# Optimization experiments

Hardware: AMD Instinct MI355X
Metric: run time of the kernel (lower is better)

Reference implementation:

```python
import jax, jax.numpy as jnp
import numpy as np

NUM_HEADS = 16


def _bayes_w(mu, rho, eps):
    # reparameterized weight sample: w = mu + softplus(rho) * eps
    return mu + jax.nn.softplus(rho) * eps


def setup_inputs() -> dict:
    key = jax.random.key(0)
    ks = jax.random.split(key, 12)
    B, N, C = 4, 2048, 1024
    x = jax.random.normal(ks[0], (B, N, C), jnp.float32)
    w_scale = 0.02
    q_w = jax.random.normal(ks[1], (C, C), jnp.float32) * w_scale
    k_w = jax.random.normal(ks[2], (C, C), jnp.float32) * w_scale
    v_mu = jax.random.normal(ks[3], (C, C), jnp.float32) * w_scale
    v_rho = jax.random.normal(ks[4], (C, C), jnp.float32) * 0.1 - 3.0
    v_eps = jax.random.normal(ks[5], (C, C), jnp.float32)
    proj_mu = jax.random.normal(ks[6], (C, C), jnp.float32) * w_scale
    proj_rho = jax.random.normal(ks[7], (C, C), jnp.float32) * 0.1 - 3.0
    proj_eps = jax.random.normal(ks[8], (C, C), jnp.float32)
    pb_mu = jax.random.normal(ks[9], (C,), jnp.float32) * w_scale
    pb_rho = jax.random.normal(ks[10], (C,), jnp.float32) * 0.1 - 3.0
    pb_eps = jax.random.normal(ks[11], (C,), jnp.float32)
    return {"x": x, "q_w": q_w, "k_w": k_w, "v_mu": v_mu, "v_rho": v_rho,
            "v_eps": v_eps, "proj_mu": proj_mu, "proj_rho": proj_rho,
            "proj_eps": proj_eps, "pb_mu": pb_mu, "pb_rho": pb_rho,
            "pb_eps": pb_eps}


def reference(x, q_w, k_w, v_mu, v_rho, v_eps, proj_mu, proj_rho, proj_eps,
              pb_mu, pb_rho, pb_eps):
    B, N, C = x.shape
    H = NUM_HEADS
    D = C // H
    scale = D ** -0.5
    v_w = _bayes_w(v_mu, v_rho, v_eps)
    # projections (torch Linear: y = x @ W.T)
    q = (x @ q_w.T).reshape(B, N, H, D).transpose(0, 2, 1, 3)  # [B,H,N,D]
    k = (x @ k_w.T).reshape(B, N, H, D).transpose(0, 2, 1, 3)
    v = (x @ v_w.T).reshape(B, N, H, D).transpose(0, 2, 1, 3)
    attn = jax.nn.softmax(jnp.einsum("bhnd,bhmd->bhnm", q * scale, k), axis=-1)
    out = jnp.einsum("bhnm,bhmd->bhnd", attn, v)
    out = out.transpose(0, 2, 1, 3).reshape(B, N, C)
    p_w = _bayes_w(proj_mu, proj_rho, proj_eps)
    p_b = _bayes_w(pb_mu, pb_rho, pb_eps)
    return out @ p_w.T + p_b
```

## Files before the change

kernel.cpp:

```cpp
#include <hip/hip_runtime.h>
#include <hip/hip_bf16.h>
#include <cstdint>
#include <math.h>

typedef __bf16 bf16;
typedef __bf16 bf16x8 __attribute__((ext_vector_type(8)));
typedef __bf16 bf16x4 __attribute__((ext_vector_type(4)));
typedef float  f32x4 __attribute__((ext_vector_type(4)));
typedef unsigned short u16x8 __attribute__((ext_vector_type(8)));

#define LOG2E 1.4426950408889634f

#define AS1 __attribute__((address_space(1)))
#define AS3 __attribute__((address_space(3)))

__device__ __forceinline__ void gload_lds16(const bf16* g, bf16* l) {
    __builtin_amdgcn_global_load_lds((AS1 void*)g, (AS3 void*)l, 16, 0, 0);
}

__device__ __forceinline__ float softplus(float r) {
    return (r > 15.f) ? r : log1pf(expf(r));
}

__global__ __launch_bounds__(256)
void cast_f32_bf16(const float* __restrict__ in, bf16* __restrict__ out, int n4) {
    int i = blockIdx.x * 256 + threadIdx.x;
    if (i < n4) {
        float4 v = ((const float4*)in)[i];
        bf16 o[4] = {(bf16)v.x, (bf16)v.y, (bf16)v.z, (bf16)v.w};
        *(uint64_t*)&out[i * 4] = *(uint64_t*)o;
    }
}

__global__ __launch_bounds__(256)
void wprep(const float* __restrict__ qw, const float* __restrict__ kw,
           const float* __restrict__ vmu, const float* __restrict__ vrho,
           const float* __restrict__ veps, bf16* __restrict__ wqkv) {
    int i = blockIdx.x * 256 + threadIdx.x;
    int r = blockIdx.y;
    float4 v;
    if (r == 0)      v = ((const float4*)qw)[i];
    else if (r == 1) v = ((const float4*)kw)[i];
    else {
        float4 m = ((const float4*)vmu)[i];
        float4 rh = ((const float4*)vrho)[i];
        float4 e = ((const float4*)veps)[i];
        v.x = m.x + softplus(rh.x) * e.x;
        v.y = m.y + softplus(rh.y) * e.y;
        v.z = m.z + softplus(rh.z) * e.z;
        v.w = m.w + softplus(rh.w) * e.w;
    }
    bf16 o[4] = {(bf16)v.x, (bf16)v.y, (bf16)v.z, (bf16)v.w};
    *(uint64_t*)&wqkv[((size_t)r << 20) + (size_t)i * 4] = *(uint64_t*)o;
}

__global__ __launch_bounds__(256)
void pprep(const float* __restrict__ pmu, const float* __restrict__ prho,
           const float* __restrict__ peps, const float* __restrict__ bmu,
           const float* __restrict__ brho, const float* __restrict__ beps,
           bf16* __restrict__ pwb, float* __restrict__ p_b) {
    int bx = blockIdx.x;
    if (bx < 1024) {
        int i = bx * 256 + threadIdx.x;
        float4 m = ((const float4*)pmu)[i];
        float4 rh = ((const float4*)prho)[i];
        float4 e = ((const float4*)peps)[i];
        bf16 o[4] = {(bf16)(m.x + softplus(rh.x) * e.x),
                     (bf16)(m.y + softplus(rh.y) * e.y),
                     (bf16)(m.z + softplus(rh.z) * e.z),
                     (bf16)(m.w + softplus(rh.w) * e.w)};
        *(uint64_t*)&pwb[(size_t)i * 4] = *(uint64_t*)o;
    } else {
        int i = threadIdx.x;
        float4 m = ((const float4*)bmu)[i];
        float4 rh = ((const float4*)brho)[i];
        float4 e = ((const float4*)beps)[i];
        float4 v = {m.x + softplus(rh.x) * e.x, m.y + softplus(rh.y) * e.y,
                    m.z + softplus(rh.z) * e.z, m.w + softplus(rh.w) * e.w};
        ((float4*)p_b)[i] = v;
    }
}

template <typename OutT>
__global__ __launch_bounds__(256)
void gemm_bt(const bf16* __restrict__ A, int lda, const bf16* __restrict__ W,
             OutT* __restrict__ C, int ldc, const float* __restrict__ bias,
             int M, int N, int K, float q_scale, int q_cols) {
    __shared__ bf16 lA[128 * 32];
    __shared__ bf16 lB[128 * 32];

    const int lane = threadIdx.x & 63;
    const int wv   = threadIdx.x >> 6;
    const int wr   = wv >> 1, wc = wv & 1;
    const int m0 = blockIdx.y * 128, n0 = blockIdx.x * 128;
    const int col = lane & 15, quad = lane >> 4;
    const float scale = (n0 < q_cols) ? q_scale : 1.0f;

    const int srow  = wv * 16 + (lane >> 2);
    const int skcol = (lane & 3) * 8;

    f32x4 acc[4][4] = {};

    for (int k0 = 0; k0 < K; k0 += 32) {
#pragma unroll
        for (int r = 0; r < 2; ++r) {
            gload_lds16(A + (size_t)(m0 + r * 64 + srow) * lda + k0 + skcol,
                        &lA[(r * 64 + wv * 16) * 32]);
            gload_lds16(W + (size_t)(n0 + r * 64 + srow) * K + k0 + skcol,
                        &lB[(r * 64 + wv * 16) * 32]);
        }
        __syncthreads();

        bf16x8 af[4], bfr[4];
#pragma unroll
        for (int t = 0; t < 4; ++t) {
            af[t]  = *(const bf16x8*)&lA[(wr * 64 + t * 16 + col) * 32 + quad * 8];
            bfr[t] = *(const bf16x8*)&lB[(wc * 64 + t * 16 + col) * 32 + quad * 8];
        }
#pragma unroll
        for (int i = 0; i < 4; ++i)
#pragma unroll
            for (int j = 0; j < 4; ++j)
                acc[i][j] = __builtin_amdgcn_mfma_f32_16x16x32_bf16(af[i], bfr[j], acc[i][j], 0, 0, 0);
        __syncthreads();
    }

#pragma unroll
    for (int i = 0; i < 4; ++i) {
        int row = m0 + wr * 64 + i * 16 + quad * 4;
#pragma unroll
        for (int j = 0; j < 4; ++j) {
            int cc = n0 + wc * 64 + j * 16 + col;
            float bv = bias ? bias[cc] : 0.f;
#pragma unroll
            for (int r = 0; r < 4; ++r)
                C[(size_t)(row + r) * ldc + cc] = (OutT)(acc[i][j][r] * scale + bv);
        }
    }
}

__global__ __launch_bounds__(256)
void vtrans(const bf16* __restrict__ QKV, bf16* __restrict__ Vt) {
    __shared__ uint32_t t[64 * 33];
    const int tid = threadIdx.x;
    const int kvt = blockIdx.x, h = blockIdx.y, b = blockIdx.z;
    const bf16* src = QKV + (size_t)(b * 2048 + kvt * 64) * 3072 + 2048 + h * 64;

    const int kp = tid >> 3, c = tid & 7;
    u16x8 v0 = *(const u16x8*)&src[(size_t)(2 * kp) * 3072 + c * 8];
    u16x8 v1 = *(const u16x8*)&src[(size_t)(2 * kp + 1) * 3072 + c * 8];
#pragma unroll
    for (int j = 0; j < 8; ++j)
        t[(c * 8 + j) * 33 + kp] = (uint32_t)v0[j] | ((uint32_t)v1[j] << 16);
    __syncthreads();

    const int d = tid >> 2, c2 = tid & 3;
    bf16* dst = &Vt[(size_t)((b * 16 + h) * 64 + d) * 2048 + kvt * 64 + c2 * 16];
    uint4 w0, w1;
    w0.x = t[d * 33 + c2 * 8 + 0];
    w0.y = t[d * 33 + c2 * 8 + 1];
    w0.z = t[d * 33 + c2 * 8 + 2];
    w0.w = t[d * 33 + c2 * 8 + 3];
    w1.x = t[d * 33 + c2 * 8 + 4];
    w1.y = t[d * 33 + c2 * 8 + 5];
    w1.z = t[d * 33 + c2 * 8 + 6];
    w1.w = t[d * 33 + c2 * 8 + 7];
    *(uint4*)dst       = w0;
    *(uint4*)(dst + 8) = w1;
}

__global__ __launch_bounds__(256, 3)
void attn_kernel(bf16* QKV, const bf16* __restrict__ Vt) {
    __shared__ bf16 sK[2][64 * 64];
    __shared__ bf16 sV[2][64 * 64];
    __shared__ bf16 sP[128 * 72];

    const int lane = threadIdx.x & 63;
    const int wv   = threadIdx.x >> 6;
    const int col  = lane & 15, quad = lane >> 4;
    const int qt = blockIdx.x, h = blockIdx.y, b = blockIdx.z;

    const size_t rowQ0 = (size_t)b * 2048 + qt * 128;
    bf16* Qg = QKV + rowQ0 * 3072 + h * 64;
    const bf16* Kg = QKV + (size_t)b * 2048 * 3072 + 1024 + h * 64;
    const bf16* Vg = Vt + (size_t)((b * 16 + h) * 64) * 2048;

    bf16x8 qf[2][2];
#pragma unroll
    for (int mi = 0; mi < 2; ++mi)
#pragma unroll
        for (int ks = 0; ks < 2; ++ks)
            qf[mi][ks] = *(const bf16x8*)&Qg[(size_t)(wv * 32 + mi * 16 + col) * 3072 + ks * 32 + quad * 8];

    const int rl = lane >> 3;
    const int cs = ((lane & 7) ^ rl) * 8;
    const bf16* Kdma = Kg + (size_t)(wv * 16 + rl) * 3072 + cs;
    const bf16* Vdma = Vg + (size_t)(wv * 16 + rl) * 2048 + cs;
    const int ldsrow = (wv * 16) * 64;

    gload_lds16(Kdma,                    &sK[0][ldsrow]);
    gload_lds16(Kdma + (size_t)8 * 3072, &sK[0][ldsrow + 8 * 64]);
    gload_lds16(Vdma,                    &sV[0][ldsrow]);
    gload_lds16(Vdma + (size_t)8 * 2048, &sV[0][ldsrow + 8 * 64]);

    f32x4 lsum[2] = {};
    f32x4 o[2][4] = {};
    const int cx = col & 7;

    for (int t = 0; t < 32; ++t) {
        __syncthreads();
        const int cur = t & 1;
        if (t < 31) {
            const int nxt = cur ^ 1;
            const size_t kvn = (size_t)(t + 1) * 64;
            gload_lds16(Kdma + kvn * 3072,       &sK[nxt][ldsrow]);
            gload_lds16(Kdma + (kvn + 8) * 3072, &sK[nxt][ldsrow + 8 * 64]);
            gload_lds16(Vdma + kvn,              &sV[nxt][ldsrow]);
            gload_lds16(Vdma + kvn + 8 * 2048,   &sV[nxt][ldsrow + 8 * 64]);
        }

        f32x4 st[2][4];
#pragma unroll
        for (int nj = 0; nj < 4; ++nj) {
            bf16x8 kf0 = *(const bf16x8*)&sK[cur][(nj * 16 + col) * 64 + ((quad ^ cx) * 8)];
            bf16x8 kf1 = *(const bf16x8*)&sK[cur][(nj * 16 + col) * 64 + (((quad ^ cx) ^ 4) * 8)];
#pragma unroll
            for (int mi = 0; mi < 2; ++mi) {
                f32x4 tt = {0.f, 0.f, 0.f, 0.f};
                tt = __builtin_amdgcn_mfma_f32_16x16x32_bf16(kf0, qf[mi][0], tt, 0, 0, 0);
                tt = __builtin_amdgcn_mfma_f32_16x16x32_bf16(kf1, qf[mi][1], tt, 0, 0, 0);
                st[mi][nj] = tt;
            }
        }

#pragma unroll
        for (int mi = 0; mi < 2; ++mi)
#pragma unroll
            for (int nj = 0; nj < 4; ++nj) {
                f32x4 p;
#pragma unroll
                for (int r = 0; r < 4; ++r) p[r] = exp2f(st[mi][nj][r]);
                lsum[mi] += p;
                bf16x4 pk = {(bf16)p[0], (bf16)p[1], (bf16)p[2], (bf16)p[3]};
                *(bf16x4*)&sP[(wv * 32 + mi * 16 + col) * 72 + nj * 16 + quad * 4] = pk;
            }

#pragma unroll
        for (int ks = 0; ks < 2; ++ks) {
            bf16x8 pf0 = *(const bf16x8*)&sP[(wv * 32 + col) * 72 + ks * 32 + quad * 8];
            bf16x8 pf1 = *(const bf16x8*)&sP[(wv * 32 + 16 + col) * 72 + ks * 32 + quad * 8];
#pragma unroll
            for (int dj = 0; dj < 4; ++dj) {
                bf16x8 vf = *(const bf16x8*)&sV[cur][(dj * 16 + col) * 64 + (((ks * 4 + quad) ^ cx) * 8)];
                o[0][dj] = __builtin_amdgcn_mfma_f32_16x16x32_bf16(pf0, vf, o[0][dj], 0, 0, 0);
                o[1][dj] = __builtin_amdgcn_mfma_f32_16x16x32_bf16(pf1, vf, o[1][dj], 0, 0, 0);
            }
        }
    }

#pragma unroll
    for (int mi = 0; mi < 2; ++mi) {
        float l = lsum[mi][0] + lsum[mi][1] + lsum[mi][2] + lsum[mi][3];
        l += __shfl_xor(l, 16, 64);
        l += __shfl_xor(l, 32, 64);
#pragma unroll
        for (int r = 0; r < 4; ++r) {
            float inv = 1.f / __shfl(l, quad * 4 + r, 64);
            int row = wv * 32 + mi * 16 + quad * 4 + r;
#pragma unroll
            for (int dj = 0; dj < 4; ++dj)
                Qg[(size_t)row * 3072 + dj * 16 + col] = (bf16)(o[mi][dj][r] * inv);
        }
    }
}

extern "C" void kernel_launch(void* const* d_in, const int* in_sizes, int n_in,
                              void* d_out, int out_size, void* d_ws, size_t ws_size,
                              hipStream_t stream) {
    const float* x      = (const float*)d_in[0];
    const float* q_w    = (const float*)d_in[1];
    const float* k_w    = (const float*)d_in[2];
    const float* v_mu   = (const float*)d_in[3];
    const float* v_rho  = (const float*)d_in[4];
    const float* v_eps  = (const float*)d_in[5];
    const float* p_mu   = (const float*)d_in[6];
    const float* p_rho  = (const float*)d_in[7];
    const float* p_eps  = (const float*)d_in[8];
    const float* pb_mu  = (const float*)d_in[9];
    const float* pb_rho = (const float*)d_in[10];
    const float* pb_eps = (const float*)d_in[11];
    float* out = (float*)d_out;

    const size_t MB = (size_t)1 << 20;
    char* ws = (char*)d_ws;
    bf16*  xb   = (bf16*)(ws);
    bf16*  wqkv = (bf16*)(ws + 16 * MB);
    bf16*  pwb  = (bf16*)(ws + 22 * MB);
    float* p_b  = (float*)(ws + 24 * MB);
    bf16*  QKV  = (bf16*)(ws + 25 * MB);
    bf16*  Vt   = xb;

    wprep<<<dim3(1024, 3), 256, 0, stream>>>(q_w, k_w, v_mu, v_rho, v_eps, wqkv);
    pprep<<<1025, 256, 0, stream>>>(p_mu, p_rho, p_eps, pb_mu, pb_rho, pb_eps, pwb, p_b);
    cast_f32_bf16<<<8192, 256, 0, stream>>>(x, xb, 2097152);

    gemm_bt<bf16><<<dim3(24, 64), 256, 0, stream>>>(xb, 1024, wqkv, QKV, 3072, nullptr,
                                                    8192, 3072, 1024, 0.125f * LOG2E, 1024);

    vtrans<<<dim3(32, 16, 4), 256, 0, stream>>>(QKV, Vt);

    attn_kernel<<<dim3(16, 16, 4), 256, 0, stream>>>(QKV, Vt);

    gemm_bt<float><<<dim3(8, 64), 256, 0, stream>>>(QKV, 3072, pwb, out, 1024, p_b,
                                                    8192, 1024, 1024, 1.0f, 0);
}
```

Measured before the change: 361.3 us.

## Switch attention to 32x32x16 MFMA and keep P in registers

Rewrites the attention inner loop to use 32x32x16 bf16 MFMA tiles instead of 16x16x32, computing S^T so each lane holds a column of probabilities. The probabilities are repacked into the PV operand with cross-half lane shuffles instead of being written to and read back from a shared-memory P buffer. This removes the sP LDS round trip and its barrier-free bank traffic, and uses a hardware exp2 intrinsic. It adds shuffle and select instructions and changes the output store pattern to scattered per-element writes.

```diff
diff --git a/kernel.cpp b/kernel.cpp
--- a/kernel.cpp
+++ b/kernel.cpp
@@ -5,11 +5,17 @@
 
 typedef __bf16 bf16;
 typedef __bf16 bf16x8 __attribute__((ext_vector_type(8)));
-typedef __bf16 bf16x4 __attribute__((ext_vector_type(4)));
-typedef float  f32x4 __attribute__((ext_vector_type(4)));
+typedef float  f32x4  __attribute__((ext_vector_type(4)));
+typedef float  f32x16 __attribute__((ext_vector_type(16)));
 typedef unsigned short u16x8 __attribute__((ext_vector_type(8)));
 
 #define LOG2E 1.4426950408889634f
+
+#if __has_builtin(__builtin_amdgcn_exp2f)
+#define EXP2(x) __builtin_amdgcn_exp2f(x)
+#else
+#define EXP2(x) exp2f(x)
+#endif
 
 #define AS1 __attribute__((address_space(1)))
 #define AS3 __attribute__((address_space(3)))
@@ -173,11 +179,11 @@
 void attn_kernel(bf16* QKV, const bf16* __restrict__ Vt) {
     __shared__ bf16 sK[2][64 * 64];
     __shared__ bf16 sV[2][64 * 64];
-    __shared__ bf16 sP[128 * 72];
 
     const int lane = threadIdx.x & 63;
     const int wv   = threadIdx.x >> 6;
-    const int col  = lane & 15, quad = lane >> 4;
+    const int r32  = lane & 31;
+    const int L    = lane >> 5;
     const int qt = blockIdx.x, h = blockIdx.y, b = blockIdx.z;
 
     const size_t rowQ0 = (size_t)b * 2048 + qt * 128;
@@ -185,12 +191,10 @@
     const bf16* Kg = QKV + (size_t)b * 2048 * 3072 + 1024 + h * 64;
     const bf16* Vg = Vt + (size_t)((b * 16 + h) * 64) * 2048;
 
-    bf16x8 qf[2][2];
-#pragma unroll
-    for (int mi = 0; mi < 2; ++mi)
-#pragma unroll
-        for (int ks = 0; ks < 2; ++ks)
-            qf[mi][ks] = *(const bf16x8*)&Qg[(size_t)(wv * 32 + mi * 16 + col) * 3072 + ks * 32 + quad * 8];
+    bf16x8 qf[4];
+#pragma unroll
+    for (int ks = 0; ks < 4; ++ks)
+        qf[ks] = *(const bf16x8*)&Qg[(size_t)(wv * 32 + r32) * 3072 + ks * 16 + L * 8];
 
     const int rl = lane >> 3;
     const int cs = ((lane & 7) ^ rl) * 8;
@@ -203,9 +207,9 @@
     gload_lds16(Vdma,                    &sV[0][ldsrow]);
     gload_lds16(Vdma + (size_t)8 * 2048, &sV[0][ldsrow + 8 * 64]);
 
-    f32x4 lsum[2] = {};
-    f32x4 o[2][4] = {};
-    const int cx = col & 7;
+    f32x16 o[2] = {};
+    float ls[4] = {};
+    const int sw7 = r32 & 7;
 
     for (int t = 0; t < 32; ++t) {
         __syncthreads();
@@ -219,58 +223,56 @@
             gload_lds16(Vdma + kvn + 8 * 2048,   &sV[nxt][ldsrow + 8 * 64]);
         }
 
-        f32x4 st[2][4];
-#pragma unroll
-        for (int nj = 0; nj < 4; ++nj) {
-            bf16x8 kf0 = *(const bf16x8*)&sK[cur][(nj * 16 + col) * 64 + ((quad ^ cx) * 8)];
-            bf16x8 kf1 = *(const bf16x8*)&sK[cur][(nj * 16 + col) * 64 + (((quad ^ cx) ^ 4) * 8)];
-#pragma unroll
-            for (int mi = 0; mi < 2; ++mi) {
-                f32x4 tt = {0.f, 0.f, 0.f, 0.f};
-                tt = __builtin_amdgcn_mfma_f32_16x16x32_bf16(kf0, qf[mi][0], tt, 0, 0, 0);
-                tt = __builtin_amdgcn_mfma_f32_16x16x32_bf16(kf1, qf[mi][1], tt, 0, 0, 0);
-                st[mi][nj] = tt;
+        f32x16 st2[2] = {};
+#pragma unroll
+        for (int ks = 0; ks < 4; ++ks) {
+            bf16x8 kf0 = *(const bf16x8*)&sK[cur][r32 * 64 + (((ks * 2 + L) ^ sw7) * 8)];
+            bf16x8 kf1 = *(const bf16x8*)&sK[cur][(32 + r32) * 64 + (((ks * 2 + L) ^ sw7) * 8)];
+            st2[0] = __builtin_amdgcn_mfma_f32_32x32x16_bf16(kf0, qf[ks], st2[0], 0, 0, 0);
+            st2[1] = __builtin_amdgcn_mfma_f32_32x32x16_bf16(kf1, qf[ks], st2[1], 0, 0, 0);
+        }
+
+        uint32_t pd[2][8];
+#pragma unroll
+        for (int kt = 0; kt < 2; ++kt)
+#pragma unroll
+            for (int p = 0; p < 8; ++p) {
+                float e0 = EXP2(st2[kt][2 * p]);
+                float e1 = EXP2(st2[kt][2 * p + 1]);
+                ls[p & 3] += e0 + e1;
+                bf16 b2[2] = {(bf16)e0, (bf16)e1};
+                pd[kt][p] = *(uint32_t*)b2;
             }
-        }
-
-#pragma unroll
-        for (int mi = 0; mi < 2; ++mi)
-#pragma unroll
-            for (int nj = 0; nj < 4; ++nj) {
-                f32x4 p;
-#pragma unroll
-                for (int r = 0; r < 4; ++r) p[r] = exp2f(st[mi][nj][r]);
-                lsum[mi] += p;
-                bf16x4 pk = {(bf16)p[0], (bf16)p[1], (bf16)p[2], (bf16)p[3]};
-                *(bf16x4*)&sP[(wv * 32 + mi * 16 + col) * 72 + nj * 16 + quad * 4] = pk;
-            }
-
-#pragma unroll
-        for (int ks = 0; ks < 2; ++ks) {
-            bf16x8 pf0 = *(const bf16x8*)&sP[(wv * 32 + col) * 72 + ks * 32 + quad * 8];
-            bf16x8 pf1 = *(const bf16x8*)&sP[(wv * 32 + 16 + col) * 72 + ks * 32 + quad * 8];
-#pragma unroll
-            for (int dj = 0; dj < 4; ++dj) {
-                bf16x8 vf = *(const bf16x8*)&sV[cur][(dj * 16 + col) * 64 + (((ks * 4 + quad) ^ cx) * 8)];
-                o[0][dj] = __builtin_amdgcn_mfma_f32_16x16x32_bf16(pf0, vf, o[0][dj], 0, 0, 0);
-                o[1][dj] = __builtin_amdgcn_mfma_f32_16x16x32_bf16(pf1, vf, o[1][dj], 0, 0, 0);
-            }
-        }
-    }
-
-#pragma unroll
-    for (int mi = 0; mi < 2; ++mi) {
-        float l = lsum[mi][0] + lsum[mi][1] + lsum[mi][2] + lsum[mi][3];
-        l += __shfl_xor(l, 16, 64);
-        l += __shfl_xor(l, 32, 64);
-#pragma unroll
-        for (int r = 0; r < 4; ++r) {
-            float inv = 1.f / __shfl(l, quad * 4 + r, 64);
-            int row = wv * 32 + mi * 16 + quad * 4 + r;
-#pragma unroll
-            for (int dj = 0; dj < 4; ++dj)
-                Qg[(size_t)row * 3072 + dj * 16 + col] = (bf16)(o[mi][dj][r] * inv);
-        }
+
+#pragma unroll
+        for (int ks = 0; ks < 4; ++ks) {
+            const int kt = ks >> 1, kb = (ks & 1) * 4;
+            uint32_t s0 = __shfl_xor((int)pd[kt][kb + 0], 32, 64);
+            uint32_t s1 = __shfl_xor((int)pd[kt][kb + 1], 32, 64);
+            uint32_t s2 = __shfl_xor((int)pd[kt][kb + 2], 32, 64);
+            uint32_t s3 = __shfl_xor((int)pd[kt][kb + 3], 32, 64);
+            union { bf16x8 v; uint32_t d[4]; } af;
+            af.d[0] = (L == 0) ? pd[kt][kb + 0] : s2;
+            af.d[1] = (L == 0) ? pd[kt][kb + 1] : s3;
+            af.d[2] = (L == 1) ? pd[kt][kb + 2] : s0;
+            af.d[3] = (L == 1) ? pd[kt][kb + 3] : s1;
+            bf16x8 vf0 = *(const bf16x8*)&sV[cur][r32 * 64 + (((ks * 2 + L) ^ sw7) * 8)];
+            bf16x8 vf1 = *(const bf16x8*)&sV[cur][(32 + r32) * 64 + (((ks * 2 + L) ^ sw7) * 8)];
+            o[0] = __builtin_amdgcn_mfma_f32_32x32x16_bf16(af.v, vf0, o[0], 0, 0, 0);
+            o[1] = __builtin_amdgcn_mfma_f32_32x32x16_bf16(af.v, vf1, o[1], 0, 0, 0);
+        }
+    }
+
+    float lsum = ls[0] + ls[1] + ls[2] + ls[3];
+    lsum += __shfl_xor(lsum, 32, 64);
+    float linv = 1.f / lsum;
+#pragma unroll
+    for (int reg = 0; reg < 16; ++reg) {
+        int qrow = (reg & 3) + 8 * (reg >> 2) + 4 * L;
+        float inv = __shfl(linv, qrow, 64);
+        size_t base = (size_t)(wv * 32 + qrow) * 3072;
+        Qg[base + r32]      = (bf16)(o[0][reg] * inv);
+        Qg[base + 32 + r32] = (bf16)(o[1][reg] * inv);
     }
 }
 
```

Result: faster. 344.1 us (-4.8%).
